# Optimization experiments

Measured on AMD Instinct MI355X. Metric: run time of the kernel, lower is better.

## Reference

```python
import jax, jax.numpy as jnp
import numpy as np

D_MODEL, D_HEAD, N_HEAD = 1024, 64, 16
B, S = 8, 1024


def setup_inputs() -> dict:
    key = jax.random.key(0)
    ks = jax.random.split(key, 11)
    sc = 1.0 / np.sqrt(D_MODEL)
    inp = {
        "query": jax.random.normal(ks[0], (B, S, D_MODEL), jnp.float32),
        "key": jax.random.normal(ks[1], (B, S, D_MODEL), jnp.float32),
        "value": jax.random.normal(ks[2], (B, S, D_MODEL), jnp.float32),
        # stacked per-head Q/K projections: [H, d_model, d_head]
        "Wq": jax.random.normal(ks[3], (N_HEAD, D_MODEL, D_HEAD), jnp.float32) * sc,
        "bq": jax.random.normal(ks[4], (N_HEAD, D_HEAD), jnp.float32) * 0.01,
        "Wk": jax.random.normal(ks[5], (N_HEAD, D_MODEL, D_HEAD), jnp.float32) * sc,
        "bk": jax.random.normal(ks[6], (N_HEAD, D_HEAD), jnp.float32) * 0.01,
        # shared V projection
        "Wv": jax.random.normal(ks[7], (D_MODEL, D_HEAD), jnp.float32) * sc,
        "bv": jax.random.normal(ks[8], (D_HEAD,), jnp.float32) * 0.01,
        # output projection d_head -> d_model
        "Wo": jax.random.normal(ks[9], (D_HEAD, D_MODEL), jnp.float32) * (1.0 / np.sqrt(D_HEAD)),
        "bo": jax.random.normal(ks[10], (D_MODEL,), jnp.float32) * 0.01,
    }
    return inp


def reference(query, key, value, Wq, bq, Wk, bk, Wv, bv, Wo, bo):
    scale = D_HEAD ** -0.5
    # per-head projections, batched over heads: [B, H, S, d_head]
    Q = jnp.einsum("bsd,hdk->bhsk", query, Wq) + bq[None, :, None, :]
    K = jnp.einsum("bsd,hdk->bhsk", key, Wk) + bk[None, :, None, :]
    # shared V: [B, S, d_head]
    V = value @ Wv + bv
    # attention weights per head: [B, H, S, S]
    wei = jax.nn.softmax(jnp.einsum("bhsk,bhtk->bhst", Q, K) * scale, axis=-1)
    # head outputs averaged (shared V): [B, S, d_head]
    out = jnp.mean(jnp.einsum("bhst,btk->bhsk", wei, V), axis=1)
    return out @ Wo + bo
```

## Files before the change

kernel.cpp:

```cpp
#include <hip/hip_runtime.h>
#include <hip/hip_bf16.h>
#include <math.h>

typedef __attribute__((ext_vector_type(4))) float  f32x4;
typedef __attribute__((ext_vector_type(8))) __bf16 bf16x8;
typedef __attribute__((ext_vector_type(4))) __bf16 bf16x4;
typedef __attribute__((ext_vector_type(4))) short  s16x4;

#define SCL 0.18033688011111543f
#define MFMA16(a, b, c)   __builtin_amdgcn_mfma_f32_16x16x32_bf16((a), (b), (c), 0, 0, 0)
#define MFMA16K16(a, b, c) __builtin_amdgcn_mfma_f32_16x16x16bf16_1k((a), (b), (c), 0, 0, 0)

union B4 { bf16x4 b; s16x4 s; };

__device__ __forceinline__ float exp2_fast(float x) {
    float r;
    asm("v_exp_f32 %0, %1" : "=v"(r) : "v"(x));
    return r;
}

__global__ __launch_bounds__(256) void pack_all(
    const float* __restrict__ Wq, const float* __restrict__ Wk,
    const float* __restrict__ Wv, const float* __restrict__ bv,
    const float* __restrict__ Wo,
    __bf16* __restrict__ WqT, __bf16* __restrict__ WkT,
    __bf16* __restrict__ WvT, float* __restrict__ bvP, __bf16* __restrict__ WoT)
{
    const int tid = threadIdx.x;
    if (blockIdx.x >= 256) {
        int idx = (blockIdx.x - 256) * 256 + tid;
        if (idx < 131072) {
            int n = idx >> 10, k = idx & 1023;
            WvT[idx] = (n < 64) ? (__bf16)Wv[k * 64 + n] : (__bf16)0.0f;
        }
        if (idx < 65536) {
            int n = idx >> 6, d = idx & 63;
            WoT[idx] = (__bf16)Wo[d * 1024 + n];
        }
        if (idx < 128) bvP[idx] = (idx < 64) ? bv[idx] : 0.0f;
        return;
    }
    __shared__ __bf16 T0[64][68];
    __shared__ __bf16 T1[64][68];
    const int h = blockIdx.x & 15, kt = blockIdx.x >> 4;
    const int kk = tid >> 2, cf = (tid & 3) * 16;
    const size_t base = (size_t)h * 65536 + (size_t)(kt * 64 + kk) * 64 + cf;
    #pragma unroll
    for (int j = 0; j < 4; ++j) {
        f32x4 v = *(const f32x4*)&Wq[base + 4 * j];
        f32x4 u = *(const f32x4*)&Wk[base + 4 * j];
        bf16x4 vb, ub;
        #pragma unroll
        for (int e = 0; e < 4; ++e) { vb[e] = (__bf16)v[e]; ub[e] = (__bf16)u[e]; }
        *(bf16x4*)&T0[kk][cf + 4 * j] = vb;
        *(bf16x4*)&T1[kk][cf + 4 * j] = ub;
    }
    __syncthreads();
    const int c = tid >> 2, k8 = (tid & 3) * 16;
    bf16x8 q0, q1, k0v, k1v;
    #pragma unroll
    for (int j = 0; j < 8; ++j) {
        q0[j] = T0[k8 + j][c];     q1[j] = T0[k8 + 8 + j][c];
        k0v[j] = T1[k8 + j][c];    k1v[j] = T1[k8 + 8 + j][c];
    }
    size_t dst = (size_t)(h * 64 + c) * 1024 + kt * 64 + k8;
    *(bf16x8*)&WqT[dst] = q0;  *(bf16x8*)&WqT[dst + 8] = q1;
    *(bf16x8*)&WkT[dst] = k0v; *(bf16x8*)&WkT[dst + 8] = k1v;
}

__global__ __launch_bounds__(256, 2) void proj_qk(
    const float* __restrict__ Aq, const float* __restrict__ Ak,
    const __bf16* __restrict__ WqT, const __bf16* __restrict__ WkT,
    const float* __restrict__ bq, const float* __restrict__ bk,
    __bf16* __restrict__ Cq, __bf16* __restrict__ Ck)
{
    const int z = blockIdx.z;
    const float* A  = z ? Ak : Aq;
    const __bf16* Bt = z ? WkT : WqT;
    const float* bias = z ? bk : bq;
    __bf16* C = z ? Ck : Cq;
    const float oscale = z ? 1.0f : SCL;

    __shared__ __bf16 As[2][128][72];
    __shared__ __bf16 Bs[2][128][72];

    const int tid = threadIdx.x;
    const int lane = tid & 63, w = tid >> 6;
    const int wr = w >> 1, wc = w & 1;
    const int l15 = lane & 15, g = lane >> 4;
    const int m0 = blockIdx.x * 128, n0 = blockIdx.y * 128;
    const int arow = tid >> 4, acf = (tid & 15) * 4;
    const int brow = tid >> 3, bc8 = (tid & 7) * 8;

    f32x4 areg[8];
    bf16x8 breg[4];
    #pragma unroll
    for (int p = 0; p < 8; ++p)
        areg[p] = *(const f32x4*)&A[(size_t)(m0 + arow + 16 * p) * 1024 + acf];
    #pragma unroll
    for (int p = 0; p < 4; ++p)
        breg[p] = *(const bf16x8*)&Bt[(size_t)(n0 + brow + 32 * p) * 1024 + bc8];

    f32x4 acc[4][4] = {};
    int cur = 0;
    for (int k0 = 0; k0 < 1024; k0 += 64) {
        #pragma unroll
        for (int p = 0; p < 8; ++p) {
            bf16x4 c4;
            #pragma unroll
            for (int e = 0; e < 4; ++e) c4[e] = (__bf16)areg[p][e];
            *(bf16x4*)&As[cur][arow + 16 * p][acf] = c4;
        }
        #pragma unroll
        for (int p = 0; p < 4; ++p)
            *(bf16x8*)&Bs[cur][brow + 32 * p][bc8] = breg[p];
        if (k0 < 960) {
            #pragma unroll
            for (int p = 0; p < 8; ++p)
                areg[p] = *(const f32x4*)&A[(size_t)(m0 + arow + 16 * p) * 1024 + k0 + 64 + acf];
            #pragma unroll
            for (int p = 0; p < 4; ++p)
                breg[p] = *(const bf16x8*)&Bt[(size_t)(n0 + brow + 32 * p) * 1024 + k0 + 64 + bc8];
        }
        __syncthreads();
        __builtin_amdgcn_s_setprio(1);
        #pragma unroll
        for (int ks = 0; ks < 2; ++ks) {
            bf16x8 af[4], bfv[4];
            #pragma unroll
            for (int mi = 0; mi < 4; ++mi)
                af[mi] = *(const bf16x8*)&As[cur][64 * wr + 16 * mi + l15][32 * ks + 8 * g];
            #pragma unroll
            for (int ni = 0; ni < 4; ++ni)
                bfv[ni] = *(const bf16x8*)&Bs[cur][64 * wc + 16 * ni + l15][32 * ks + 8 * g];
            #pragma unroll
            for (int mi = 0; mi < 4; ++mi)
                #pragma unroll
                for (int ni = 0; ni < 4; ++ni)
                    acc[mi][ni] = MFMA16(af[mi], bfv[ni], acc[mi][ni]);
        }
        __builtin_amdgcn_s_setprio(0);
        cur ^= 1;
    }

    #pragma unroll
    for (int mi = 0; mi < 4; ++mi)
        #pragma unroll
        for (int ni = 0; ni < 4; ++ni) {
            int n = n0 + 64 * wc + 16 * ni + l15;
            float bn = bias[n];
            #pragma unroll
            for (int r = 0; r < 4; ++r) {
                int m = m0 + 64 * wr + 16 * mi + 4 * g + r;
                C[(size_t)m * 1024 + n] = (__bf16)((acc[mi][ni][r] + bn) * oscale);
            }
        }
}

__global__ __launch_bounds__(256, 2) void proj_v(
    const float* __restrict__ A, const __bf16* __restrict__ Bt,
    const float* __restrict__ bias, __bf16* __restrict__ C)
{
    __shared__ __bf16 As[2][64][72];
    __shared__ __bf16 Bs[2][64][72];

    const int tid = threadIdx.x;
    const int lane = tid & 63, w = tid >> 6;
    const int wr = w >> 1, wc = w & 1;
    const int l15 = lane & 15, g = lane >> 4;
    const int m0 = blockIdx.x * 64;
    const int arow = tid >> 2, acf = (tid & 3) * 16;
    const int bcf = (tid & 3) * 16;

    f32x4 areg[4];
    bf16x8 breg[2];
    #pragma unroll
    for (int j = 0; j < 4; ++j)
        areg[j] = *(const f32x4*)&A[(size_t)(m0 + arow) * 1024 + acf + 4 * j];
    #pragma unroll
    for (int j = 0; j < 2; ++j)
        breg[j] = *(const bf16x8*)&Bt[(size_t)arow * 1024 + bcf + 8 * j];

    f32x4 acc[2][2] = {};
    int cur = 0;
    for (int k0 = 0; k0 < 1024; k0 += 64) {
        #pragma unroll
        for (int j = 0; j < 4; ++j) {
            bf16x4 c4;
            #pragma unroll
            for (int e = 0; e < 4; ++e) c4[e] = (__bf16)areg[j][e];
            *(bf16x4*)&As[cur][arow][acf + 4 * j] = c4;
        }
        #pragma unroll
        for (int j = 0; j < 2; ++j)
            *(bf16x8*)&Bs[cur][arow][bcf + 8 * j] = breg[j];
        if (k0 < 960) {
            #pragma unroll
            for (int j = 0; j < 4; ++j)
                areg[j] = *(const f32x4*)&A[(size_t)(m0 + arow) * 1024 + k0 + 64 + acf + 4 * j];
            #pragma unroll
            for (int j = 0; j < 2; ++j)
                breg[j] = *(const bf16x8*)&Bt[(size_t)arow * 1024 + k0 + 64 + bcf + 8 * j];
        }
        __syncthreads();
        #pragma unroll
        for (int ks = 0; ks < 2; ++ks) {
            bf16x8 af[2], bfv[2];
            #pragma unroll
            for (int mi = 0; mi < 2; ++mi)
                af[mi] = *(const bf16x8*)&As[cur][32 * wr + 16 * mi + l15][32 * ks + 8 * g];
            #pragma unroll
            for (int ni = 0; ni < 2; ++ni)
                bfv[ni] = *(const bf16x8*)&Bs[cur][32 * wc + 16 * ni + l15][32 * ks + 8 * g];
            #pragma unroll
            for (int mi = 0; mi < 2; ++mi)
                #pragma unroll
                for (int ni = 0; ni < 2; ++ni)
                    acc[mi][ni] = MFMA16(af[mi], bfv[ni], acc[mi][ni]);
        }
        __syncthreads();
        cur ^= 1;
    }

    #pragma unroll
    for (int mi = 0; mi < 2; ++mi)
        #pragma unroll
        for (int ni = 0; ni < 2; ++ni) {
            int n = 32 * wc + 16 * ni + l15;
            float bn = bias[n];
            #pragma unroll
            for (int r = 0; r < 4; ++r) {
                int m = m0 + 32 * wr + 16 * mi + 4 * g + r;
                C[(size_t)n * 8192 + m] = (__bf16)(acc[mi][ni][r] + bn);
            }
        }
}

__global__ __launch_bounds__(128, 4) void attn_kernel(
    const __bf16* __restrict__ Qb, const __bf16* __restrict__ Kb,
    const __bf16* __restrict__ Vt, __bf16* __restrict__ Oh)
{
    __shared__ __bf16 Ks[2][32][68];
    __shared__ __bf16 Vs[2][64][44];

    const int qt = blockIdx.x, bh = blockIdx.y;
    const int b = bh >> 4, h = bh & 15;
    const int tid = threadIdx.x;
    const int lane = tid & 63, w = tid >> 6;
    const int l15 = lane & 15, g = lane >> 4;
    const int s0 = b * 1024 + qt * 64;

    const int krow = tid >> 2, kc = (tid & 3) * 16;
    const int vrow = tid >> 1, vc = (tid & 1) * 16;

    bf16x8 qf[2][2];
    #pragma unroll
    for (int mi = 0; mi < 2; ++mi)
        #pragma unroll
        for (int ks = 0; ks < 2; ++ks)
            qf[mi][ks] = *(const bf16x8*)
                &Qb[(size_t)(s0 + 32 * w + 16 * mi + l15) * 1024 + h * 64 + 32 * ks + 8 * g];

    const __bf16* Kbase = Kb + (size_t)(b * 1024) * 1024 + h * 64;
    const __bf16* Vbase = Vt + (size_t)b * 1024;

    bf16x8 kreg[2], vreg[2];
    #pragma unroll
    for (int j = 0; j < 2; ++j) {
        kreg[j] = *(const bf16x8*)&Kbase[(size_t)krow * 1024 + kc + 8 * j];
        vreg[j] = *(const bf16x8*)&Vbase[(size_t)vrow * 8192 + vc + 8 * j];
    }

    f32x4 acc_o[2][4] = {};
    float l_par[2] = {0.0f, 0.0f};

    int cur = 0;
    for (int it = 0; it < 32; ++it) {
        *(bf16x8*)&Ks[cur][krow][kc]     = kreg[0];
        *(bf16x8*)&Ks[cur][krow][kc + 8] = kreg[1];
        *(bf16x8*)&Vs[cur][vrow][vc]     = vreg[0];
        *(bf16x8*)&Vs[cur][vrow][vc + 8] = vreg[1];
        if (it < 31) {
            int t1 = (it + 1) * 32;
            #pragma unroll
            for (int j = 0; j < 2; ++j) {
                kreg[j] = *(const bf16x8*)&Kbase[(size_t)(t1 + krow) * 1024 + kc + 8 * j];
                vreg[j] = *(const bf16x8*)&Vbase[(size_t)vrow * 8192 + t1 + vc + 8 * j];
            }
        }
        __syncthreads();

        f32x4 pacc[2][2] = {};
        __builtin_amdgcn_s_setprio(1);
        #pragma unroll
        for (int ks = 0; ks < 2; ++ks) {
            bf16x8 kf[2];
            #pragma unroll
            for (int ni = 0; ni < 2; ++ni)
                kf[ni] = *(const bf16x8*)&Ks[cur][16 * ni + l15][32 * ks + 8 * g];
            #pragma unroll
            for (int mi = 0; mi < 2; ++mi)
                #pragma unroll
                for (int ni = 0; ni < 2; ++ni)
                    pacc[mi][ni] = MFMA16(kf[ni], qf[mi][ks], pacc[mi][ni]);
        }
        __builtin_amdgcn_s_setprio(0);

        s16x4 pb[2][2];
        #pragma unroll
        for (int mi = 0; mi < 2; ++mi) {
            float rs = 0.0f;
            #pragma unroll
            for (int ni = 0; ni < 2; ++ni) {
                B4 pk;
                #pragma unroll
                for (int r = 0; r < 4; ++r) {
                    float pv = exp2_fast(pacc[mi][ni][r]);
                    rs += pv;
                    pk.b[r] = (__bf16)pv;
                }
                pb[mi][ni] = pk.s;
            }
            l_par[mi] += rs;
        }

        __builtin_amdgcn_s_setprio(1);
        #pragma unroll
        for (int c = 0; c < 2; ++c) {
            s16x4 vf[4];
            #pragma unroll
            for (int nd = 0; nd < 4; ++nd) {
                B4 vv;
                vv.b = *(const bf16x4*)&Vs[cur][16 * nd + l15][16 * c + 4 * g];
                vf[nd] = vv.s;
            }
            #pragma unroll
            for (int mi = 0; mi < 2; ++mi)
                #pragma unroll
                for (int nd = 0; nd < 4; ++nd)
                    acc_o[mi][nd] = MFMA16K16(vf[nd], pb[mi][c], acc_o[mi][nd]);
        }
        __builtin_amdgcn_s_setprio(0);
        cur ^= 1;
    }

    #pragma unroll
    for (int mi = 0; mi < 2; ++mi) {
        float l = l_par[mi];
        l += __shfl_xor(l, 16);
        l += __shfl_xor(l, 32);
        float rl = 1.0f / l;
        int q = qt * 64 + 32 * w + 16 * mi + l15;
        #pragma unroll
        for (int nd = 0; nd < 4; ++nd) {
            bf16x4 ov;
            #pragma unroll
            for (int r = 0; r < 4; ++r) ov[r] = (__bf16)(acc_o[mi][nd][r] * rl);
            *(bf16x4*)&Oh[(size_t)(bh * 1024 + q) * 64 + 16 * nd + 4 * g] = ov;
        }
    }
}

__global__ __launch_bounds__(256) void mean_kernel(
    const __bf16* __restrict__ Oh, __bf16* __restrict__ Om)
{
    int idx = blockIdx.x * 256 + threadIdx.x;
    int m = idx >> 3, d8 = (idx & 7) * 8;
    int b = m >> 10, q = m & 1023;
    const __bf16* src = Oh + (size_t)(b * 16) * 65536 + (size_t)q * 64 + d8;
    float s[8] = {};
    #pragma unroll
    for (int h = 0; h < 16; ++h) {
        bf16x8 v = *(const bf16x8*)&src[(size_t)h * 65536];
        #pragma unroll
        for (int j = 0; j < 8; ++j) s[j] += (float)v[j];
    }
    bf16x8 o;
    #pragma unroll
    for (int j = 0; j < 8; ++j) o[j] = (__bf16)(s[j] * 0.0625f);
    *(bf16x8*)&Om[(size_t)m * 64 + d8] = o;
}

__global__ __launch_bounds__(256, 4) void out_gemm(
    const __bf16* __restrict__ Om, const __bf16* __restrict__ WoT,
    const float* __restrict__ bo, float* __restrict__ out)
{
    const int tid = threadIdx.x;
    const int lane = tid & 63, w = tid >> 6;
    const int wr = w >> 1, wc = w & 1;
    const int l15 = lane & 15, g = lane >> 4;
    const int m0 = blockIdx.x * 128, n0 = blockIdx.y * 128;

    f32x4 acc[4][4] = {};
    #pragma unroll
    for (int ks = 0; ks < 2; ++ks) {
        bf16x8 af[4], bfv[4];
        #pragma unroll
        for (int mi = 0; mi < 4; ++mi)
            af[mi] = *(const bf16x8*)&Om[(size_t)(m0 + 64 * wr + 16 * mi + l15) * 64 + 32 * ks + 8 * g];
        #pragma unroll
        for (int ni = 0; ni < 4; ++ni)
            bfv[ni] = *(const bf16x8*)&WoT[(size_t)(n0 + 64 * wc + 16 * ni + l15) * 64 + 32 * ks + 8 * g];
        #pragma unroll
        for (int mi = 0; mi < 4; ++mi)
            #pragma unroll
            for (int ni = 0; ni < 4; ++ni)
                acc[mi][ni] = MFMA16(af[mi], bfv[ni], acc[mi][ni]);
    }
    #pragma unroll
    for (int mi = 0; mi < 4; ++mi)
        #pragma unroll
        for (int ni = 0; ni < 4; ++ni) {
            int n = n0 + 64 * wc + 16 * ni + l15;
            float bn = bo[n];
            #pragma unroll
            for (int r = 0; r < 4; ++r) {
                int m = m0 + 64 * wr + 16 * mi + 4 * g + r;
                out[(size_t)m * 1024 + n] = acc[mi][ni][r] + bn;
            }
        }
}

extern "C" void kernel_launch(void* const* d_in, const int* in_sizes, int n_in,
                              void* d_out, int out_size, void* d_ws, size_t ws_size,
                              hipStream_t stream)
{
    const float* query = (const float*)d_in[0];
    const float* key_  = (const float*)d_in[1];
    const float* value = (const float*)d_in[2];
    const float* Wq = (const float*)d_in[3];
    const float* bq = (const float*)d_in[4];
    const float* Wk = (const float*)d_in[5];
    const float* bk = (const float*)d_in[6];
    const float* Wv = (const float*)d_in[7];
    const float* bv = (const float*)d_in[8];
    const float* Wo = (const float*)d_in[9];
    const float* bo = (const float*)d_in[10];
    float* out = (float*)d_out;

    char* p = (char*)d_ws;
    __bf16* Qbuf = (__bf16*)p; p += 8192ull * 1024 * 2;
    __bf16* Kbuf = (__bf16*)p; p += 8192ull * 1024 * 2;
    __bf16* VtB  = (__bf16*)p; p += 64ull * 8192 * 2;
    __bf16* WqT  = (__bf16*)p; p += 1024ull * 1024 * 2;
    __bf16* WkT  = (__bf16*)p; p += 1024ull * 1024 * 2;
    __bf16* WvT  = (__bf16*)p; p += 128ull * 1024 * 2;
    __bf16* WoT  = (__bf16*)p; p += 1024ull * 64 * 2;
    float*  bvP  = (float*)p;  p += 128 * 4;
    __bf16* Oh   = (__bf16*)p; p += 8ull * 16 * 1024 * 64 * 2;
    __bf16* Om   = (__bf16*)p; p += 8192ull * 64 * 2;

    pack_all<<<768, 256, 0, stream>>>(Wq, Wk, Wv, bv, Wo, WqT, WkT, WvT, bvP, WoT);
    proj_qk<<<dim3(64, 8, 2), 256, 0, stream>>>(query, key_, WqT, WkT, bq, bk, Qbuf, Kbuf);
    proj_v<<<128, 256, 0, stream>>>(value, WvT, bvP, VtB);
    attn_kernel<<<dim3(16, 128), 128, 0, stream>>>(Qbuf, Kbuf, VtB, Oh);
    mean_kernel<<<256, 256, 0, stream>>>(Oh, Om);
    out_gemm<<<dim3(64, 8), 256, 0, stream>>>(Om, WoT, bo, out);
}
```

Before: 140.5 us.

## Pre-convert Q/K inputs to bf16 and use direct global-to-LDS loads in proj_qk

Adds a separate kernel that converts the fp32 query and key activations to bf16. proj_qk then streams bf16 tiles straight into LDS with global_load_lds, using an XOR-swizzled layout instead of padded rows, and single-buffers the tiles so it can run 4 blocks per CU. The aim is to drop the register round-trip and the in-loop fp32-to-bf16 conversion and to raise occupancy. In exchange it adds an extra pass that reads 64MB and writes 32MB, a second barrier per k-step, and loses the register-prefetch double buffering.

```diff
diff --git a/kernel.cpp b/kernel.cpp
--- a/kernel.cpp
+++ b/kernel.cpp
@@ -17,6 +17,12 @@
     float r;
     asm("v_exp_f32 %0, %1" : "=v"(r) : "v"(x));
     return r;
+}
+
+__device__ __forceinline__ void gload16(const __bf16* g, __bf16* l) {
+    __builtin_amdgcn_global_load_lds(
+        (const __attribute__((address_space(1))) void*)g,
+        (__attribute__((address_space(3))) void*)l, 16, 0, 0);
 }
 
 __global__ __launch_bounds__(256) void pack_all(
@@ -68,71 +74,78 @@
     *(bf16x8*)&WkT[dst] = k0v; *(bf16x8*)&WkT[dst + 8] = k1v;
 }
 
-__global__ __launch_bounds__(256, 2) void proj_qk(
-    const float* __restrict__ Aq, const float* __restrict__ Ak,
+__global__ __launch_bounds__(256) void cvt2(
+    const float* __restrict__ q, const float* __restrict__ k,
+    __bf16* __restrict__ qb, __bf16* __restrict__ kb)
+{
+    size_t base = ((size_t)blockIdx.x * 256 + threadIdx.x) * 8;
+    f32x4 a0 = *(const f32x4*)&q[base];
+    f32x4 a1 = *(const f32x4*)&q[base + 4];
+    f32x4 b0 = *(const f32x4*)&k[base];
+    f32x4 b1 = *(const f32x4*)&k[base + 4];
+    bf16x8 oq, ok;
+    #pragma unroll
+    for (int j = 0; j < 4; ++j) {
+        oq[j] = (__bf16)a0[j]; oq[4 + j] = (__bf16)a1[j];
+        ok[j] = (__bf16)b0[j]; ok[4 + j] = (__bf16)b1[j];
+    }
+    *(bf16x8*)&qb[base] = oq;
+    *(bf16x8*)&kb[base] = ok;
+}
+
+__global__ __launch_bounds__(256, 4) void proj_qk(
+    const __bf16* __restrict__ Aq, const __bf16* __restrict__ Ak,
     const __bf16* __restrict__ WqT, const __bf16* __restrict__ WkT,
     const float* __restrict__ bq, const float* __restrict__ bk,
     __bf16* __restrict__ Cq, __bf16* __restrict__ Ck)
 {
     const int z = blockIdx.z;
-    const float* A  = z ? Ak : Aq;
+    const __bf16* A  = z ? Ak : Aq;
     const __bf16* Bt = z ? WkT : WqT;
     const float* bias = z ? bk : bq;
     __bf16* C = z ? Ck : Cq;
     const float oscale = z ? 1.0f : SCL;
 
-    __shared__ __bf16 As[2][128][72];
-    __shared__ __bf16 Bs[2][128][72];
+    __shared__ __bf16 As[128][64];
+    __shared__ __bf16 Bs[128][64];
 
     const int tid = threadIdx.x;
     const int lane = tid & 63, w = tid >> 6;
     const int wr = w >> 1, wc = w & 1;
     const int l15 = lane & 15, g = lane >> 4;
     const int m0 = blockIdx.x * 128, n0 = blockIdx.y * 128;
-    const int arow = tid >> 4, acf = (tid & 15) * 4;
-    const int brow = tid >> 3, bc8 = (tid & 7) * 8;
-
-    f32x4 areg[8];
-    bf16x8 breg[4];
-    #pragma unroll
-    for (int p = 0; p < 8; ++p)
-        areg[p] = *(const f32x4*)&A[(size_t)(m0 + arow + 16 * p) * 1024 + acf];
-    #pragma unroll
-    for (int p = 0; p < 4; ++p)
-        breg[p] = *(const bf16x8*)&Bt[(size_t)(n0 + brow + 32 * p) * 1024 + bc8];
+
+    const int lrow8 = lane >> 3;
+    const int slot  = (lane & 7) ^ lrow8;
+    const int scol  = slot * 8;
 
     f32x4 acc[4][4] = {};
-    int cur = 0;
+
     for (int k0 = 0; k0 < 1024; k0 += 64) {
         #pragma unroll
-        for (int p = 0; p < 8; ++p) {
-            bf16x4 c4;
-            #pragma unroll
-            for (int e = 0; e < 4; ++e) c4[e] = (__bf16)areg[p][e];
-            *(bf16x4*)&As[cur][arow + 16 * p][acf] = c4;
-        }
-        #pragma unroll
-        for (int p = 0; p < 4; ++p)
-            *(bf16x8*)&Bs[cur][brow + 32 * p][bc8] = breg[p];
-        if (k0 < 960) {
-            #pragma unroll
-            for (int p = 0; p < 8; ++p)
-                areg[p] = *(const f32x4*)&A[(size_t)(m0 + arow + 16 * p) * 1024 + k0 + 64 + acf];
-            #pragma unroll
-            for (int p = 0; p < 4; ++p)
-                breg[p] = *(const bf16x8*)&Bt[(size_t)(n0 + brow + 32 * p) * 1024 + k0 + 64 + bc8];
+        for (int c = 0; c < 4; ++c) {
+            int row = w * 32 + c * 8 + lrow8;
+            gload16(&A [(size_t)(m0 + row) * 1024 + k0 + scol], &As[0][0] + (w * 4 + c) * 512);
+            gload16(&Bt[(size_t)(n0 + row) * 1024 + k0 + scol], &Bs[0][0] + (w * 4 + c) * 512);
         }
         __syncthreads();
+
         __builtin_amdgcn_s_setprio(1);
         #pragma unroll
         for (int ks = 0; ks < 2; ++ks) {
             bf16x8 af[4], bfv[4];
             #pragma unroll
-            for (int mi = 0; mi < 4; ++mi)
-                af[mi] = *(const bf16x8*)&As[cur][64 * wr + 16 * mi + l15][32 * ks + 8 * g];
-            #pragma unroll
-            for (int ni = 0; ni < 4; ++ni)
-                bfv[ni] = *(const bf16x8*)&Bs[cur][64 * wc + 16 * ni + l15][32 * ks + 8 * g];
+            for (int mi = 0; mi < 4; ++mi) {
+                int row = 64 * wr + 16 * mi + l15;
+                af[mi] = *(const bf16x8*)((const char*)&As[0][0]
+                            + row * 128 + (((4 * ks + g) ^ (row & 7)) << 4));
+            }
+            #pragma unroll
+            for (int ni = 0; ni < 4; ++ni) {
+                int row = 64 * wc + 16 * ni + l15;
+                bfv[ni] = *(const bf16x8*)((const char*)&Bs[0][0]
+                            + row * 128 + (((4 * ks + g) ^ (row & 7)) << 4));
+            }
             #pragma unroll
             for (int mi = 0; mi < 4; ++mi)
                 #pragma unroll
@@ -140,7 +153,7 @@
                     acc[mi][ni] = MFMA16(af[mi], bfv[ni], acc[mi][ni]);
         }
         __builtin_amdgcn_s_setprio(0);
-        cur ^= 1;
+        __syncthreads();
     }
 
     #pragma unroll
@@ -449,9 +462,12 @@
     float*  bvP  = (float*)p;  p += 128 * 4;
     __bf16* Oh   = (__bf16*)p; p += 8ull * 16 * 1024 * 64 * 2;
     __bf16* Om   = (__bf16*)p; p += 8192ull * 64 * 2;
+    __bf16* Qa   = (__bf16*)p; p += 8192ull * 1024 * 2;
+    __bf16* Ka   = (__bf16*)p; p += 8192ull * 1024 * 2;
 
     pack_all<<<768, 256, 0, stream>>>(Wq, Wk, Wv, bv, Wo, WqT, WkT, WvT, bvP, WoT);
-    proj_qk<<<dim3(64, 8, 2), 256, 0, stream>>>(query, key_, WqT, WkT, bq, bk, Qbuf, Kbuf);
+    cvt2<<<4096, 256, 0, stream>>>(query, key_, Qa, Ka);
+    proj_qk<<<dim3(64, 8, 2), 256, 0, stream>>>(Qa, Ka, WqT, WkT, bq, bk, Qbuf, Kbuf);
     proj_v<<<128, 256, 0, stream>>>(value, WvT, bvP, VtB);
     attn_kernel<<<dim3(16, 128), 128, 0, stream>>>(Qbuf, Kbuf, VtB, Oh);
     mean_kernel<<<256, 256, 0, stream>>>(Oh, Om);
```

New measurement: 143.8 us. 1.02x slower.

## Software-pipeline attention loop: overlap QK of next tile with PV of previous

Applied to the files above, without the earlier changes.

Restructures the attention inner loop so K is prefetched two tiles ahead and the P·V MFMAs for tile it-1 are issued right after the QK MFMAs for tile it. The exp/softmax step then overlaps with matrix work, and the PV epilogue for the last tile is moved after the loop. The goal is to hide exp latency and the barrier stall behind tensor-core work. The cost is extra register pressure from keeping pb live across iterations, plus more complex buffer indexing with a single barrier per iteration.

```diff
diff --git a/kernel.cpp b/kernel.cpp
--- a/kernel.cpp
+++ b/kernel.cpp
@@ -266,29 +266,41 @@
 
     bf16x8 kreg[2], vreg[2];
     #pragma unroll
+    for (int j = 0; j < 2; ++j)
+        kreg[j] = *(const bf16x8*)&Kbase[(size_t)krow * 1024 + kc + 8 * j];
+    *(bf16x8*)&Ks[0][krow][kc]     = kreg[0];
+    *(bf16x8*)&Ks[0][krow][kc + 8] = kreg[1];
+    #pragma unroll
     for (int j = 0; j < 2; ++j) {
-        kreg[j] = *(const bf16x8*)&Kbase[(size_t)krow * 1024 + kc + 8 * j];
+        kreg[j] = *(const bf16x8*)&Kbase[(size_t)(32 + krow) * 1024 + kc + 8 * j];
         vreg[j] = *(const bf16x8*)&Vbase[(size_t)vrow * 8192 + vc + 8 * j];
     }
+    __syncthreads();
 
     f32x4 acc_o[2][4] = {};
     float l_par[2] = {0.0f, 0.0f};
-
-    int cur = 0;
+    s16x4 pb[2][2];
+
     for (int it = 0; it < 32; ++it) {
-        *(bf16x8*)&Ks[cur][krow][kc]     = kreg[0];
-        *(bf16x8*)&Ks[cur][krow][kc + 8] = kreg[1];
+        const int cur = it & 1;
+        if (it < 31) {
+            *(bf16x8*)&Ks[cur ^ 1][krow][kc]     = kreg[0];
+            *(bf16x8*)&Ks[cur ^ 1][krow][kc + 8] = kreg[1];
+        }
         *(bf16x8*)&Vs[cur][vrow][vc]     = vreg[0];
         *(bf16x8*)&Vs[cur][vrow][vc + 8] = vreg[1];
+        if (it < 30) {
+            int t2 = (it + 2) * 32;
+            #pragma unroll
+            for (int j = 0; j < 2; ++j)
+                kreg[j] = *(const bf16x8*)&Kbase[(size_t)(t2 + krow) * 1024 + kc + 8 * j];
+        }
         if (it < 31) {
             int t1 = (it + 1) * 32;
             #pragma unroll
-            for (int j = 0; j < 2; ++j) {
-                kreg[j] = *(const bf16x8*)&Kbase[(size_t)(t1 + krow) * 1024 + kc + 8 * j];
+            for (int j = 0; j < 2; ++j)
                 vreg[j] = *(const bf16x8*)&Vbase[(size_t)vrow * 8192 + t1 + vc + 8 * j];
-            }
-        }
-        __syncthreads();
+        }
 
         f32x4 pacc[2][2] = {};
         __builtin_amdgcn_s_setprio(1);
@@ -304,9 +316,25 @@
                 for (int ni = 0; ni < 2; ++ni)
                     pacc[mi][ni] = MFMA16(kf[ni], qf[mi][ks], pacc[mi][ni]);
         }
+        if (it > 0) {
+            #pragma unroll
+            for (int c = 0; c < 2; ++c) {
+                s16x4 vf[4];
+                #pragma unroll
+                for (int nd = 0; nd < 4; ++nd) {
+                    B4 vv;
+                    vv.b = *(const bf16x4*)&Vs[cur ^ 1][16 * nd + l15][16 * c + 4 * g];
+                    vf[nd] = vv.s;
+                }
+                #pragma unroll
+                for (int mi = 0; mi < 2; ++mi)
+                    #pragma unroll
+                    for (int nd = 0; nd < 4; ++nd)
+                        acc_o[mi][nd] = MFMA16K16(vf[nd], pb[mi][c], acc_o[mi][nd]);
+            }
+        }
         __builtin_amdgcn_s_setprio(0);
 
-        s16x4 pb[2][2];
         #pragma unroll
         for (int mi = 0; mi < 2; ++mi) {
             float rs = 0.0f;
@@ -323,26 +351,26 @@
             }
             l_par[mi] += rs;
         }
-
-        __builtin_amdgcn_s_setprio(1);
-        #pragma unroll
-        for (int c = 0; c < 2; ++c) {
-            s16x4 vf[4];
-            #pragma unroll
-            for (int nd = 0; nd < 4; ++nd) {
-                B4 vv;
-                vv.b = *(const bf16x4*)&Vs[cur][16 * nd + l15][16 * c + 4 * g];
-                vf[nd] = vv.s;
-            }
-            #pragma unroll
-            for (int mi = 0; mi < 2; ++mi)
-                #pragma unroll
-                for (int nd = 0; nd < 4; ++nd)
-                    acc_o[mi][nd] = MFMA16K16(vf[nd], pb[mi][c], acc_o[mi][nd]);
-        }
-        __builtin_amdgcn_s_setprio(0);
-        cur ^= 1;
-    }
+        __syncthreads();
+    }
+
+    __builtin_amdgcn_s_setprio(1);
+    #pragma unroll
+    for (int c = 0; c < 2; ++c) {
+        s16x4 vf[4];
+        #pragma unroll
+        for (int nd = 0; nd < 4; ++nd) {
+            B4 vv;
+            vv.b = *(const bf16x4*)&Vs[1][16 * nd + l15][16 * c + 4 * g];
+            vf[nd] = vv.s;
+        }
+        #pragma unroll
+        for (int mi = 0; mi < 2; ++mi)
+            #pragma unroll
+            for (int nd = 0; nd < 4; ++nd)
+                acc_o[mi][nd] = MFMA16K16(vf[nd], pb[mi][c], acc_o[mi][nd]);
+    }
+    __builtin_amdgcn_s_setprio(0);
 
     #pragma unroll
     for (int mi = 0; mi < 2; ++mi) {
```

Measured after the change: 141.3 us. About the same (+0.5%).
